# Optimization experiments

Measured on AMD Instinct MI355X. Metric: run time of the kernel, lower is better.

The kernel has to match this reference:

```python
import jax, jax.numpy as jnp
import numpy as np

N_NODES = 100000
N_EDGES = 600000
F_IN, HID, CLS = 128, 128, 16


def sage_conv(x, src, dst, W_l, b_l, W_r, n_nodes):
    # mean aggregation of neighbor features: message x[src] scattered to dst
    msg = x[src]                                              # [E, F]
    agg = jax.ops.segment_sum(msg, dst, num_segments=n_nodes)  # [N, F]
    deg = jax.ops.segment_sum(jnp.ones((src.shape[0],), x.dtype), dst, num_segments=n_nodes)
    agg = agg / jnp.maximum(deg, 1.0)[:, None]
    # PyG SAGEConv: lin_l(agg) (with bias) + lin_r(x_root) (no bias)
    return agg @ W_l + b_l + x @ W_r


def setup_inputs() -> dict:
    key = jax.random.key(0)
    ks = jax.random.split(key, 6)
    x = jax.random.normal(ks[0], (N_NODES, F_IN), jnp.float32)
    edge_index = jax.random.randint(ks[1], (2, N_EDGES), 0, N_NODES, dtype=jnp.int64)
    s1 = 1.0 / np.sqrt(F_IN)
    s2 = 1.0 / np.sqrt(HID)
    return {
        "x": x,
        "edge_index": edge_index,
        "W1_l": jax.random.normal(ks[2], (F_IN, HID), jnp.float32) * s1,
        "b1": jnp.zeros((HID,), jnp.float32),
        "W1_r": jax.random.normal(ks[3], (F_IN, HID), jnp.float32) * s1,
        "W2_l": jax.random.normal(ks[4], (HID, CLS), jnp.float32) * s2,
        "b2": jnp.zeros((CLS,), jnp.float32),
        "W2_r": jax.random.normal(ks[5], (HID, CLS), jnp.float32) * s2,
    }


def reference(x, edge_index, W1_l, b1, W1_r, W2_l, b2, W2_r):
    n = x.shape[0]
    src, dst = edge_index[0], edge_index[1]
    h = sage_conv(x, src, dst, W1_l, b1, W1_r, n)
    h = jax.nn.relu(h)
    # F.dropout(training=self.training): identity in eval mode
    out = sage_conv(h, src, dst, W2_l, b2, W2_r, n)
    return jax.nn.log_softmax(out, axis=1)
```

## Files before the change

### kernel.cpp

```cpp
#include <hip/hip_runtime.h>
#include <cstdint>

#define N_NODES 100000
#define N_PAD 100096
#define N_EDGES 600000
#define F 128
#define CLS 16
#define CAP 32

typedef short bf16x8 __attribute__((ext_vector_type(8)));
typedef float f32x4 __attribute__((ext_vector_type(4)));

__device__ inline float bf2f(unsigned int lo16) { return __uint_as_float(lo16 << 16); }
__device__ inline unsigned short f2b(float f) {
    unsigned int u = __float_as_uint(f);
    return (unsigned short)((u + 0x7fffu + ((u >> 16) & 1u)) >> 16);
}

__global__ __launch_bounds__(256) void prep_k(const int* __restrict__ src,
                                              const int* __restrict__ dst,
                                              int* __restrict__ deg,
                                              int* __restrict__ bucket,
                                              const float* __restrict__ x,
                                              unsigned short* __restrict__ xb,
                                              const float* __restrict__ W1l,
                                              const float* __restrict__ W1r,
                                              const float* __restrict__ W2l,
                                              const float* __restrict__ W2r,
                                              unsigned short* __restrict__ w1t,
                                              unsigned short* __restrict__ w2t) {
    int b = blockIdx.x;
    if (b < 2344) {
        int e = b * 256 + threadIdx.x;
        if (e < N_EDGES) {
            int d = dst[e];
            int slot = atomicAdd(&deg[d], 1);
            if (slot < CAP) bucket[d * CAP + slot] = src[e];
        }
    } else if (b < 14844) {
        int i = (b - 2344) * 256 + threadIdx.x;
        float4 v = ((const float4*)x)[i];
        ushort4 o;
        o.x = f2b(v.x); o.y = f2b(v.y); o.z = f2b(v.z); o.w = f2b(v.w);
        ((ushort4*)xb)[i] = o;
    } else if (b < 14972) {
        int idx = (b - 14844) * 256 + threadIdx.x;
        int n = idx >> 8, k = idx & 255;
        float v = (k < F) ? W1l[k * F + n] : W1r[(k - F) * F + n];
        int ct = n >> 4, m = n & 15;
        int half = k >> 7, ks = (k >> 5) & 3, quad = (k >> 3) & 3, j = k & 7;
        w1t[(ct * 8 + ks * 2 + half) * 512 + (quad * 16 + m) * 8 + j] = f2b(v);
    } else {
        int idx = (b - 14972) * 256 + threadIdx.x;
        if (idx < 32 * F) {
            int n = idx >> 7, k = idx & 127;
            float v = (n < CLS) ? W2l[k * CLS + n] : W2r[k * CLS + (n - CLS)];
            int tile = n >> 4, m = n & 15;
            int ks = (k >> 5) & 3, quad = (k >> 3) & 3, j = k & 7;
            w2t[(tile * 4 + ks) * 512 + (quad * 16 + m) * 8 + j] = f2b(v);
        }
    }
}

__global__ __launch_bounds__(256) void gemm_fused(const unsigned short* __restrict__ Xb,
                                                  const int* __restrict__ deg,
                                                  const int* __restrict__ bucket,
                                                  const unsigned short* __restrict__ Wt,
                                                  const float* __restrict__ bias,
                                                  const unsigned short* __restrict__ Wt2,
                                                  unsigned short* __restrict__ trLb,
                                                  float* __restrict__ trR) {
    __shared__ unsigned short sh[128 * 136];
    int tid = threadIdx.x;
    int row0 = blockIdx.x * 128;

    uint4 pwm0, pwm1, pwm2, pwm3, pwm4, pwm5, pwm6, pwm7;
    {
        const uint4* xb4 = (const uint4*)Xb + (size_t)blockIdx.x * 2048 + tid;
        pwm0 = xb4[0 * 256]; pwm1 = xb4[1 * 256]; pwm2 = xb4[2 * 256]; pwm3 = xb4[3 * 256];
        pwm4 = xb4[4 * 256]; pwm5 = xb4[5 * 256]; pwm6 = xb4[6 * 256]; pwm7 = xb4[7 * 256];
    }

    {
        int ns = tid >> 1, half = tid & 1;
        const int4* gsrc = (const int4*)(bucket + (size_t)(row0 + ns) * CAP + half * 16);
        int* drow = (int*)(sh + ns * 136);
        int4* ldst = (int4*)(drow + half * 16);
        ldst[0] = gsrc[0];
        ldst[1] = gsrc[1];
        ldst[2] = gsrc[2];
        ldst[3] = gsrc[3];
        if (half == 0) drow[32] = deg[row0 + ns];
    }
    asm volatile("" :: "v"(pwm0.x), "v"(pwm1.x), "v"(pwm2.x), "v"(pwm3.x),
                       "v"(pwm4.x), "v"(pwm5.x), "v"(pwm6.x), "v"(pwm7.x));

    int grp = tid >> 4, l16 = tid & 15, f8 = l16 * 8;
    int lrb = grp * 8;

#define ISSUE(P, DV, LR) do { \
    const int* brow_ = (const int*)(sh + (LR) * 136); \
    int node_ = row0 + (LR); \
    int draw_ = brow_[32]; \
    DV = (node_ < N_NODES) ? min(max(draw_, 0), CAP) : 0; \
    int4 b0_ = ((const int4*)brow_)[0]; \
    int4 b1_ = ((const int4*)brow_)[1]; \
    int4 b2_ = ((const int4*)brow_)[2]; \
    int n0_  = (DV > 0 ) ? min(max(b0_.x, 0), N_NODES - 1) : 0; \
    int n1_  = (DV > 1 ) ? min(max(b0_.y, 0), N_NODES - 1) : 0; \
    int n2_  = (DV > 2 ) ? min(max(b0_.z, 0), N_NODES - 1) : 0; \
    int n3_  = (DV > 3 ) ? min(max(b0_.w, 0), N_NODES - 1) : 0; \
    int n4_  = (DV > 4 ) ? min(max(b1_.x, 0), N_NODES - 1) : 0; \
    int n5_  = (DV > 5 ) ? min(max(b1_.y, 0), N_NODES - 1) : 0; \
    int n6_  = (DV > 6 ) ? min(max(b1_.z, 0), N_NODES - 1) : 0; \
    int n7_  = (DV > 7 ) ? min(max(b1_.w, 0), N_NODES - 1) : 0; \
    int n8_  = (DV > 8 ) ? min(max(b2_.x, 0), N_NODES - 1) : 0; \
    int n9_  = (DV > 9 ) ? min(max(b2_.y, 0), N_NODES - 1) : 0; \
    int n10_ = (DV > 10) ? min(max(b2_.z, 0), N_NODES - 1) : 0; \
    int n11_ = (DV > 11) ? min(max(b2_.w, 0), N_NODES - 1) : 0; \
    P##0  = *(const uint4*)(Xb + (size_t)n0_  * F + f8); \
    P##1  = *(const uint4*)(Xb + (size_t)n1_  * F + f8); \
    P##2  = *(const uint4*)(Xb + (size_t)n2_  * F + f8); \
    P##3  = *(const uint4*)(Xb + (size_t)n3_  * F + f8); \
    P##4  = *(const uint4*)(Xb + (size_t)n4_  * F + f8); \
    P##5  = *(const uint4*)(Xb + (size_t)n5_  * F + f8); \
    P##6  = *(const uint4*)(Xb + (size_t)n6_  * F + f8); \
    P##7  = *(const uint4*)(Xb + (size_t)n7_  * F + f8); \
    P##8  = *(const uint4*)(Xb + (size_t)n8_  * F + f8); \
    P##9  = *(const uint4*)(Xb + (size_t)n9_  * F + f8); \
    P##10 = *(const uint4*)(Xb + (size_t)n10_ * F + f8); \
    P##11 = *(const uint4*)(Xb + (size_t)n11_ * F + f8); \
} while (0)

#define ACC8(vv) { \
    acc_[0] += bf2f((vv).x & 0xffffu); acc_[1] += bf2f((vv).x >> 16); \
    acc_[2] += bf2f((vv).y & 0xffffu); acc_[3] += bf2f((vv).y >> 16); \
    acc_[4] += bf2f((vv).z & 0xffffu); acc_[5] += bf2f((vv).z >> 16); \
    acc_[6] += bf2f((vv).w & 0xffffu); acc_[7] += bf2f((vv).w >> 16); }

#define CONSUME(P, DV, LR) do { \
    float acc_[8] = {0.f, 0.f, 0.f, 0.f, 0.f, 0.f, 0.f, 0.f}; \
    if (DV > 0)  ACC8(P##0); \
    if (DV > 1)  ACC8(P##1); \
    if (DV > 2)  ACC8(P##2); \
    if (DV > 3)  ACC8(P##3); \
    if (DV > 4)  ACC8(P##4); \
    if (DV > 5)  ACC8(P##5); \
    if (DV > 6)  ACC8(P##6); \
    if (DV > 7)  ACC8(P##7); \
    if (DV > 8)  ACC8(P##8); \
    if (DV > 9)  ACC8(P##9); \
    if (DV > 10) ACC8(P##10); \
    if (DV > 11) ACC8(P##11); \
    if (DV > 12) { \
        const int* brow_ = (const int*)(sh + (LR) * 136); \
        for (int j0 = 12; j0 < DV; j0 += 4) { \
            int4 bb_ = *(const int4*)(brow_ + j0); \
            int rem_ = DV - j0; \
            int m0_ = (rem_ > 0) ? min(max(bb_.x, 0), N_NODES - 1) : 0; \
            int m1_ = (rem_ > 1) ? min(max(bb_.y, 0), N_NODES - 1) : 0; \
            int m2_ = (rem_ > 2) ? min(max(bb_.z, 0), N_NODES - 1) : 0; \
            int m3_ = (rem_ > 3) ? min(max(bb_.w, 0), N_NODES - 1) : 0; \
            uint4 w0_ = *(const uint4*)(Xb + (size_t)m0_ * F + f8); \
            uint4 w1_ = *(const uint4*)(Xb + (size_t)m1_ * F + f8); \
            uint4 w2_ = *(const uint4*)(Xb + (size_t)m2_ * F + f8); \
            uint4 w3_ = *(const uint4*)(Xb + (size_t)m3_ * F + f8); \
            if (rem_ > 0) ACC8(w0_); \
            if (rem_ > 1) ACC8(w1_); \
            if (rem_ > 2) ACC8(w2_); \
            if (rem_ > 3) ACC8(w3_); \
        } \
    } \
    float inv_ = 1.0f / fmaxf((float)DV, 1.0f); \
    uint4 o_; \
    o_.x = (unsigned int)f2b(acc_[0] * inv_) | ((unsigned int)f2b(acc_[1] * inv_) << 16); \
    o_.y = (unsigned int)f2b(acc_[2] * inv_) | ((unsigned int)f2b(acc_[3] * inv_) << 16); \
    o_.z = (unsigned int)f2b(acc_[4] * inv_) | ((unsigned int)f2b(acc_[5] * inv_) << 16); \
    o_.w = (unsigned int)f2b(acc_[6] * inv_) | ((unsigned int)f2b(acc_[7] * inv_) << 16); \
    *(uint4*)&sh[(LR) * 136 + f8] = o_; \
} while (0)

    {
        uint4 vA0, vA1, vA2, vA3, vA4, vA5, vA6, vA7, vA8, vA9, vA10, vA11;
        uint4 vB0, vB1, vB2, vB3, vB4, vB5, vB6, vB7, vB8, vB9, vB10, vB11;
        int dA, dB;
        ISSUE(vA, dA, lrb + 0);
        ISSUE(vB, dB, lrb + 1);
        CONSUME(vA, dA, lrb + 0);
        ISSUE(vA, dA, lrb + 2);
        CONSUME(vB, dB, lrb + 1);
        ISSUE(vB, dB, lrb + 3);
        CONSUME(vA, dA, lrb + 2);
        ISSUE(vA, dA, lrb + 4);
        CONSUME(vB, dB, lrb + 3);
        ISSUE(vB, dB, lrb + 5);
        CONSUME(vA, dA, lrb + 4);
        ISSUE(vA, dA, lrb + 6);
        CONSUME(vB, dB, lrb + 5);
        ISSUE(vB, dB, lrb + 7);
        CONSUME(vA, dA, lrb + 6);
        CONSUME(vB, dB, lrb + 7);
    }
#undef ISSUE
#undef ACC8
#undef CONSUME
    __syncthreads();

    int wave = tid >> 6, lane = tid & 63;
    int m = lane & 15, quad = lane >> 4;
    int koff = quad * 8;
    int wrow0 = row0 + wave * 32;

    const unsigned short* sa0 = sh + (wave * 32 + m) * 136 + koff;
    const unsigned short* sa1 = sa0 + 16 * 136;
    const unsigned short* px0 = Xb + (size_t)(wrow0 + m) * F + koff;
    const unsigned short* px1 = px0 + 16 * F;
    const unsigned short* pw = Wt + lane * 8;

    f32x4 acc0[8], acc1[8];
#pragma unroll
    for (int ct = 0; ct < 8; ct++) { acc0[ct] = (f32x4){0,0,0,0}; acc1[ct] = (f32x4){0,0,0,0}; }

#pragma unroll
    for (int ks = 0; ks < 4; ks++) {
        bf16x8 a0 = *(const bf16x8*)(const void*)(sa0 + ks * 32);
        bf16x8 a1 = *(const bf16x8*)(const void*)(sa1 + ks * 32);
        bf16x8 x0 = *(const bf16x8*)(const void*)(px0 + ks * 32);
        bf16x8 x1 = *(const bf16x8*)(const void*)(px1 + ks * 32);
#pragma unroll
        for (int ct = 0; ct < 8; ct++) {
            bf16x8 bl = *(const bf16x8*)(const void*)(pw + (ct * 8 + ks * 2 + 0) * 512);
            bf16x8 br = *(const bf16x8*)(const void*)(pw + (ct * 8 + ks * 2 + 1) * 512);
            acc0[ct] = __builtin_amdgcn_mfma_f32_16x16x32_bf16(a0, bl, acc0[ct], 0, 0, 0);
            acc1[ct] = __builtin_amdgcn_mfma_f32_16x16x32_bf16(a1, bl, acc1[ct], 0, 0, 0);
            acc0[ct] = __builtin_amdgcn_mfma_f32_16x16x32_bf16(x0, br, acc0[ct], 0, 0, 0);
            acc1[ct] = __builtin_amdgcn_mfma_f32_16x16x32_bf16(x1, br, acc1[ct], 0, 0, 0);
        }
    }
    __syncthreads();

    int lr0 = wave * 32 + quad * 4;
#pragma unroll
    for (int ct = 0; ct < 8; ct++) {
        int n = ct * 16 + m;
        float bv = bias[n];
#pragma unroll
        for (int r = 0; r < 4; r++) {
            sh[(lr0 + r) * 136 + n]      = f2b(fmaxf(acc0[ct][r] + bv, 0.f));
            sh[(lr0 + 16 + r) * 136 + n] = f2b(fmaxf(acc1[ct][r] + bv, 0.f));
        }
    }
    __syncthreads();

    const unsigned short* hl0 = sh + (wave * 32 + m) * 136 + koff;
    const unsigned short* hl1 = hl0 + 16 * 136;
    const unsigned short* pw2 = Wt2 + lane * 8;

    f32x4 al0 = (f32x4){0,0,0,0}, al1 = (f32x4){0,0,0,0};
    f32x4 ar0 = (f32x4){0,0,0,0}, ar1 = (f32x4){0,0,0,0};
#pragma unroll
    for (int ks = 0; ks < 4; ks++) {
        bf16x8 h0 = *(const bf16x8*)(const void*)(hl0 + ks * 32);
        bf16x8 h1 = *(const bf16x8*)(const void*)(hl1 + ks * 32);
        bf16x8 wl = *(const bf16x8*)(const void*)(pw2 + (0 * 4 + ks) * 512);
        bf16x8 wr = *(const bf16x8*)(const void*)(pw2 + (1 * 4 + ks) * 512);
        al0 = __builtin_amdgcn_mfma_f32_16x16x32_bf16(h0, wl, al0, 0, 0, 0);
        al1 = __builtin_amdgcn_mfma_f32_16x16x32_bf16(h1, wl, al1, 0, 0, 0);
        ar0 = __builtin_amdgcn_mfma_f32_16x16x32_bf16(h0, wr, ar0, 0, 0, 0);
        ar1 = __builtin_amdgcn_mfma_f32_16x16x32_bf16(h1, wr, ar1, 0, 0, 0);
    }
    int r0 = wrow0 + quad * 4;
#pragma unroll
    for (int r = 0; r < 4; r++) {
        trLb[(size_t)(r0 + r) * CLS + m]      = f2b(al0[r]);
        trLb[(size_t)(r0 + 16 + r) * CLS + m] = f2b(al1[r]);
        trR[(size_t)(r0 + r) * CLS + m]       = ar0[r];
        trR[(size_t)(r0 + 16 + r) * CLS + m]  = ar1[r];
    }
}

__global__ __launch_bounds__(256) void agg2sm_k(const unsigned short* __restrict__ trLb,
                                                const float* __restrict__ trR,
                                                const int* __restrict__ deg,
                                                const int* __restrict__ bucket,
                                                const float* __restrict__ b2,
                                                float* __restrict__ out) {
    int node = blockIdx.x * 4 + (threadIdx.x >> 6);
    int lane = threadIdx.x & 63;
    int r = lane >> 2;
    int cq = (lane & 3) * 4;
    const int* bk = bucket + node * CAP;

    int d_raw = deg[node];
    int d = min(d_raw, CAP);
    int nb = (r < d) ? min(max(bk[r], 0), N_NODES - 1) : 0;
    uint2 v = *(const uint2*)(trLb + (size_t)nb * CLS + cq);
    float4 selfR = *(const float4*)(trR + (size_t)node * CLS + cq);

    float4 acc = {0.f, 0.f, 0.f, 0.f};
    if (r < d) {
        acc.x += bf2f(v.x & 0xffffu); acc.y += bf2f(v.x >> 16);
        acc.z += bf2f(v.y & 0xffffu); acc.w += bf2f(v.y >> 16);
    }
    if (d > 16) {
        int idx = 16 + r;
        bool valid = idx < d;
        int m2 = valid ? min(max(bk[idx], 0), N_NODES - 1) : 0;
        uint2 w = *(const uint2*)(trLb + (size_t)m2 * CLS + cq);
        if (valid) {
            acc.x += bf2f(w.x & 0xffffu); acc.y += bf2f(w.x >> 16);
            acc.z += bf2f(w.y & 0xffffu); acc.w += bf2f(w.y >> 16);
        }
    }
#pragma unroll
    for (int off = 4; off <= 32; off <<= 1) {
        acc.x += __shfl_xor(acc.x, off);
        acc.y += __shfl_xor(acc.y, off);
        acc.z += __shfl_xor(acc.z, off);
        acc.w += __shfl_xor(acc.w, off);
    }
    float inv = 1.0f / fmaxf((float)d, 1.0f);
    float4 bb = *(const float4*)(b2 + cq);
    float vx = acc.x * inv + selfR.x + bb.x;
    float vy = acc.y * inv + selfR.y + bb.y;
    float vz = acc.z * inv + selfR.z + bb.z;
    float vw = acc.w * inv + selfR.w + bb.w;
    float mx = fmaxf(fmaxf(vx, vy), fmaxf(vz, vw));
    mx = fmaxf(mx, __shfl_xor(mx, 1));
    mx = fmaxf(mx, __shfl_xor(mx, 2));
    float sm = __expf(vx - mx) + __expf(vy - mx) + __expf(vz - mx) + __expf(vw - mx);
    sm += __shfl_xor(sm, 1);
    sm += __shfl_xor(sm, 2);
    float lg = __logf(sm);
    if (r == 0) {
        float4 o = {vx - mx - lg, vy - mx - lg, vz - mx - lg, vw - mx - lg};
        *(float4*)(out + (size_t)node * CLS + cq) = o;
    }
}


extern "C" void kernel_launch(void* const* d_in, const int* in_sizes, int n_in,
                              void* d_out, int out_size, void* d_ws, size_t ws_size,
                              hipStream_t stream) {
    const float* x   = (const float*)d_in[0];
    const int*   ei  = (const int*)d_in[1];
    const float* W1l = (const float*)d_in[2];
    const float* b1  = (const float*)d_in[3];
    const float* W1r = (const float*)d_in[4];
    const float* W2l = (const float*)d_in[5];
    const float* b2  = (const float*)d_in[6];
    const float* W2r = (const float*)d_in[7];
    float* out = (float*)d_out;

    const int* src = ei;
    const int* dst = ei + N_EDGES;

    char* ws = (char*)d_ws;
    size_t off = 0;
    auto alloc = [&](size_t bytes) { char* p = ws + off; off += (bytes + 127) / 128 * 128; return p; };
    int* deg    = (int*)alloc((size_t)N_NODES * 4);
    int* bucket = (int*)alloc((size_t)N_NODES * CAP * 4);
    unsigned short* xb   = (unsigned short*)alloc((size_t)N_PAD * F * 2);
    unsigned short* trLb = (unsigned short*)alloc((size_t)N_PAD * CLS * 2);
    float*          trR  = (float*)alloc((size_t)N_PAD * CLS * 4);
    unsigned short* w1t  = (unsigned short*)alloc((size_t)F * 256 * 2);
    unsigned short* w2t  = (unsigned short*)alloc((size_t)32 * F * 2);

    (void)hipMemsetAsync(deg, 0, (size_t)N_NODES * 4, stream);
    prep_k<<<14988, 256, 0, stream>>>(src, dst, deg, bucket, x, xb,
                                      W1l, W1r, W2l, W2r, w1t, w2t);
    gemm_fused<<<N_PAD / 128, 256, 0, stream>>>(xb, deg, bucket, w1t, b1, w2t, trLb, trR);
    agg2sm_k<<<N_NODES / 4, 256, 0, stream>>>(trLb, trR, deg, bucket, b2, out);
}
```

Before: 212.8 us.

## Halve gemm_fused row tile to 64 and drop the Xb prefetch

The fused aggregate+GEMM kernel now handles 64 rows per block instead of 128, so each wave gathers 4 rows and computes one 16-row MFMA tile instead of two. This doubles the block count and halves shared memory per block, aiming for more occupancy and better latency hiding on the gather-heavy phase. The explicit prefetch of the block's Xb rows into registers is removed. In exchange, each W1/W2 weight fragment load is reused across half as many rows, and the gather pipeline per thread is shorter.

```diff
diff --git a/kernel.cpp b/kernel.cpp
--- a/kernel.cpp
+++ b/kernel.cpp
@@ -70,33 +70,22 @@
                                                   const unsigned short* __restrict__ Wt2,
                                                   unsigned short* __restrict__ trLb,
                                                   float* __restrict__ trR) {
-    __shared__ unsigned short sh[128 * 136];
+    __shared__ unsigned short sh[64 * 136];
     int tid = threadIdx.x;
-    int row0 = blockIdx.x * 128;
-
-    uint4 pwm0, pwm1, pwm2, pwm3, pwm4, pwm5, pwm6, pwm7;
+    int row0 = blockIdx.x * 64;
+
     {
-        const uint4* xb4 = (const uint4*)Xb + (size_t)blockIdx.x * 2048 + tid;
-        pwm0 = xb4[0 * 256]; pwm1 = xb4[1 * 256]; pwm2 = xb4[2 * 256]; pwm3 = xb4[3 * 256];
-        pwm4 = xb4[4 * 256]; pwm5 = xb4[5 * 256]; pwm6 = xb4[6 * 256]; pwm7 = xb4[7 * 256];
-    }
-
-    {
-        int ns = tid >> 1, half = tid & 1;
-        const int4* gsrc = (const int4*)(bucket + (size_t)(row0 + ns) * CAP + half * 16);
+        int ns = tid >> 2, q = tid & 3;
+        const int4* gsrc = (const int4*)(bucket + (size_t)(row0 + ns) * CAP + q * 8);
         int* drow = (int*)(sh + ns * 136);
-        int4* ldst = (int4*)(drow + half * 16);
+        int4* ldst = (int4*)(drow + q * 8);
         ldst[0] = gsrc[0];
         ldst[1] = gsrc[1];
-        ldst[2] = gsrc[2];
-        ldst[3] = gsrc[3];
-        if (half == 0) drow[32] = deg[row0 + ns];
-    }
-    asm volatile("" :: "v"(pwm0.x), "v"(pwm1.x), "v"(pwm2.x), "v"(pwm3.x),
-                       "v"(pwm4.x), "v"(pwm5.x), "v"(pwm6.x), "v"(pwm7.x));
+        if (q == 0) drow[32] = deg[row0 + ns];
+    }
 
     int grp = tid >> 4, l16 = tid & 15, f8 = l16 * 8;
-    int lrb = grp * 8;
+    int lrb = grp * 4;
 
 #define ISSUE(P, DV, LR) do { \
     const int* brow_ = (const int*)(sh + (LR) * 136); \
@@ -191,15 +180,7 @@
         CONSUME(vB, dB, lrb + 1);
         ISSUE(vB, dB, lrb + 3);
         CONSUME(vA, dA, lrb + 2);
-        ISSUE(vA, dA, lrb + 4);
         CONSUME(vB, dB, lrb + 3);
-        ISSUE(vB, dB, lrb + 5);
-        CONSUME(vA, dA, lrb + 4);
-        ISSUE(vA, dA, lrb + 6);
-        CONSUME(vB, dB, lrb + 5);
-        ISSUE(vB, dB, lrb + 7);
-        CONSUME(vA, dA, lrb + 6);
-        CONSUME(vB, dB, lrb + 7);
     }
 #undef ISSUE
 #undef ACC8
@@ -209,73 +190,59 @@
     int wave = tid >> 6, lane = tid & 63;
     int m = lane & 15, quad = lane >> 4;
     int koff = quad * 8;
-    int wrow0 = row0 + wave * 32;
-
-    const unsigned short* sa0 = sh + (wave * 32 + m) * 136 + koff;
-    const unsigned short* sa1 = sa0 + 16 * 136;
+    int wrow0 = row0 + wave * 16;
+
+    const unsigned short* sa0 = sh + (wave * 16 + m) * 136 + koff;
     const unsigned short* px0 = Xb + (size_t)(wrow0 + m) * F + koff;
-    const unsigned short* px1 = px0 + 16 * F;
     const unsigned short* pw = Wt + lane * 8;
 
-    f32x4 acc0[8], acc1[8];
-#pragma unroll
-    for (int ct = 0; ct < 8; ct++) { acc0[ct] = (f32x4){0,0,0,0}; acc1[ct] = (f32x4){0,0,0,0}; }
+    f32x4 acc0[8];
+#pragma unroll
+    for (int ct = 0; ct < 8; ct++) acc0[ct] = (f32x4){0, 0, 0, 0};
 
 #pragma unroll
     for (int ks = 0; ks < 4; ks++) {
         bf16x8 a0 = *(const bf16x8*)(const void*)(sa0 + ks * 32);
-        bf16x8 a1 = *(const bf16x8*)(const void*)(sa1 + ks * 32);
         bf16x8 x0 = *(const bf16x8*)(const void*)(px0 + ks * 32);
-        bf16x8 x1 = *(const bf16x8*)(const void*)(px1 + ks * 32);
 #pragma unroll
         for (int ct = 0; ct < 8; ct++) {
             bf16x8 bl = *(const bf16x8*)(const void*)(pw + (ct * 8 + ks * 2 + 0) * 512);
             bf16x8 br = *(const bf16x8*)(const void*)(pw + (ct * 8 + ks * 2 + 1) * 512);
             acc0[ct] = __builtin_amdgcn_mfma_f32_16x16x32_bf16(a0, bl, acc0[ct], 0, 0, 0);
-            acc1[ct] = __builtin_amdgcn_mfma_f32_16x16x32_bf16(a1, bl, acc1[ct], 0, 0, 0);
             acc0[ct] = __builtin_amdgcn_mfma_f32_16x16x32_bf16(x0, br, acc0[ct], 0, 0, 0);
-            acc1[ct] = __builtin_amdgcn_mfma_f32_16x16x32_bf16(x1, br, acc1[ct], 0, 0, 0);
         }
     }
     __syncthreads();
 
-    int lr0 = wave * 32 + quad * 4;
+    int lr0 = wave * 16 + quad * 4;
 #pragma unroll
     for (int ct = 0; ct < 8; ct++) {
         int n = ct * 16 + m;
         float bv = bias[n];
 #pragma unroll
-        for (int r = 0; r < 4; r++) {
-            sh[(lr0 + r) * 136 + n]      = f2b(fmaxf(acc0[ct][r] + bv, 0.f));
-            sh[(lr0 + 16 + r) * 136 + n] = f2b(fmaxf(acc1[ct][r] + bv, 0.f));
-        }
+        for (int r = 0; r < 4; r++)
+            sh[(lr0 + r) * 136 + n] = f2b(fmaxf(acc0[ct][r] + bv, 0.f));
     }
     __syncthreads();
 
-    const unsigned short* hl0 = sh + (wave * 32 + m) * 136 + koff;
-    const unsigned short* hl1 = hl0 + 16 * 136;
+    const unsigned short* hl0 = sh + (wave * 16 + m) * 136 + koff;
     const unsigned short* pw2 = Wt2 + lane * 8;
 
-    f32x4 al0 = (f32x4){0,0,0,0}, al1 = (f32x4){0,0,0,0};
-    f32x4 ar0 = (f32x4){0,0,0,0}, ar1 = (f32x4){0,0,0,0};
+    f32x4 al0 = (f32x4){0, 0, 0, 0};
+    f32x4 ar0 = (f32x4){0, 0, 0, 0};
 #pragma unroll
     for (int ks = 0; ks < 4; ks++) {
         bf16x8 h0 = *(const bf16x8*)(const void*)(hl0 + ks * 32);
-        bf16x8 h1 = *(const bf16x8*)(const void*)(hl1 + ks * 32);
         bf16x8 wl = *(const bf16x8*)(const void*)(pw2 + (0 * 4 + ks) * 512);
         bf16x8 wr = *(const bf16x8*)(const void*)(pw2 + (1 * 4 + ks) * 512);
         al0 = __builtin_amdgcn_mfma_f32_16x16x32_bf16(h0, wl, al0, 0, 0, 0);
-        al1 = __builtin_amdgcn_mfma_f32_16x16x32_bf16(h1, wl, al1, 0, 0, 0);
         ar0 = __builtin_amdgcn_mfma_f32_16x16x32_bf16(h0, wr, ar0, 0, 0, 0);
-        ar1 = __builtin_amdgcn_mfma_f32_16x16x32_bf16(h1, wr, ar1, 0, 0, 0);
     }
     int r0 = wrow0 + quad * 4;
 #pragma unroll
     for (int r = 0; r < 4; r++) {
-        trLb[(size_t)(r0 + r) * CLS + m]      = f2b(al0[r]);
-        trLb[(size_t)(r0 + 16 + r) * CLS + m] = f2b(al1[r]);
-        trR[(size_t)(r0 + r) * CLS + m]       = ar0[r];
-        trR[(size_t)(r0 + 16 + r) * CLS + m]  = ar1[r];
+        trLb[(size_t)(r0 + r) * CLS + m] = f2b(al0[r]);
+        trR[(size_t)(r0 + r) * CLS + m]  = ar0[r];
     }
 }
 
@@ -369,6 +336,6 @@
     (void)hipMemsetAsync(deg, 0, (size_t)N_NODES * 4, stream);
     prep_k<<<14988, 256, 0, stream>>>(src, dst, deg, bucket, x, xb,
                                       W1l, W1r, W2l, W2r, w1t, w2t);
-    gemm_fused<<<N_PAD / 128, 256, 0, stream>>>(xb, deg, bucket, w1t, b1, w2t, trLb, trR);
+    gemm_fused<<<N_PAD / 64, 256, 0, stream>>>(xb, deg, bucket, w1t, b1, w2t, trLb, trR);
     agg2sm_k<<<N_NODES / 4, 256, 0, stream>>>(trLb, trR, deg, bucket, b2, out);
 }
```

After: 212.5 us. Within noise of the previous version (-0.2%).
